# Optimization experiments

Hardware: AMD Instinct MI355X
Metric: run time of the kernel (lower is better)

## Reference

```python
import jax, jax.numpy as jnp
import numpy as np

B, T, D, H, LAT = 64, 512, 128, 512, 128


def setup_inputs() -> dict:
    key = jax.random.key(0)
    ks = jax.random.split(key, 17)
    s = lambda k, shape: (jax.random.normal(k, shape, jnp.float32) * 0.05)
    return {
        "padded_input": jax.random.normal(ks[0], (B, T, D), jnp.float32),
        "lengths": jnp.full((B,), T, jnp.int32),  # full lengths: packed == padded
        "W_ih_f": s(ks[1], (4 * H, D)), "W_hh_f": s(ks[2], (4 * H, H)), "b_f": s(ks[3], (4 * H,)),
        "W_ih_b": s(ks[4], (4 * H, D)), "W_hh_b": s(ks[5], (4 * H, H)), "b_b": s(ks[6], (4 * H,)),
        "W_ih_d": s(ks[7], (4 * H, D)), "W_hh_d": s(ks[8], (4 * H, H)), "b_d": s(ks[9], (4 * H,)),
        "W_lat": s(ks[10], (LAT, 4 * H)), "b_lat": s(ks[11], (LAT,)),
        "W_l2h": s(ks[12], (H, LAT)), "b_l2h": s(ks[13], (H,)),
        "W_out": s(ks[14], (D, H)), "b_out": s(ks[15], (D,)),
        "skip_alpha": jnp.asarray(0.5, jnp.float32),
    }


def _lstm(x, W_ih, W_hh, b, h0, c0):
    # x: [B, T, Din]; PyTorch gate order i, f, g, o; b = b_ih + b_hh pre-summed.
    xg = jnp.einsum('btd,gd->tbg', x, W_ih) + b  # [T, B, 4H], input GEMM hoisted out of scan

    def step(carry, xg_t):
        h, c = carry
        g = xg_t + h @ W_hh.T
        i, f, gc, o = jnp.split(g, 4, axis=-1)
        c = jax.nn.sigmoid(f) * c + jax.nn.sigmoid(i) * jnp.tanh(gc)
        h = jax.nn.sigmoid(o) * jnp.tanh(c)
        return (h, c), h

    (hT, cT), ys = jax.lax.scan(step, (h0, c0), xg)
    return jnp.transpose(ys, (1, 0, 2)), hT, cT  # [B, T, H], final h, final c


def reference(padded_input, lengths, W_ih_f, W_hh_f, b_f, W_ih_b, W_hh_b, b_b,
              W_ih_d, W_hh_d, b_d, W_lat, b_lat, W_l2h, b_l2h, W_out, b_out, skip_alpha):
    Bz, Tz, _ = padded_input.shape
    dt = padded_input.dtype
    z0 = jnp.zeros((Bz, H), dt)

    # Bidirectional encoder (single layer)
    out_f, hf, _ = _lstm(padded_input, W_ih_f, W_hh_f, b_f, z0, z0)
    out_b_rev, hb, _ = _lstm(padded_input[:, ::-1, :], W_ih_b, W_hh_b, b_b, z0, z0)
    out_b = out_b_rev[:, ::-1, :]
    enc_out = jnp.concatenate([out_f, out_b], axis=-1)  # [B, T, 2H]
    h_cat = jnp.concatenate([hf, hb], axis=-1)          # [B, 2H]

    # Masked mean pooling over valid timesteps
    mask = (jnp.arange(Tz)[None, :] < lengths[:, None]).astype(dt)[..., None]
    mean_hidden = (enc_out * mask).sum(axis=1) / lengths[:, None].astype(dt)
    latent_input = jnp.concatenate([h_cat, mean_hidden], axis=-1)  # [B, 4H]
    latent = latent_input @ W_lat.T + b_lat

    # Decoder init from latent; c0 = zeros
    h_dec = latent @ W_l2h.T + b_l2h

    # Teacher forcing with ratio 1.0, eval dropout, no noise:
    # per-step loop == one LSTM over padded_input[:, :T-1]
    dec_in = padded_input[:, :Tz - 1, :]
    y, _, _ = _lstm(dec_in, W_ih_d, W_hh_d, b_d, h_dec, jnp.zeros_like(h_dec))
    decoded = jnp.einsum('bth,dh->btd', y, W_out) + b_out  # [B, T-1, D]

    alpha = jax.nn.sigmoid(skip_alpha)
    return alpha * decoded + (1.0 - alpha) * padded_input[:, 1:, :]
```

## Files before the change

kernel.cpp:

```cpp
#include <hip/hip_runtime.h>
#include <cstdint>
#include <cstddef>

typedef __attribute__((ext_vector_type(8))) short bf16x8;
typedef __attribute__((ext_vector_type(4))) float f32x4;
typedef __attribute__((ext_vector_type(4))) unsigned u32x4;
typedef __attribute__((ext_vector_type(2))) unsigned u32x2;
typedef unsigned short ushort_t;

constexpr int kB = 64;
constexpr int kT = 512;
constexpr int kD = 128;
constexpr int kH = 512;
constexpr int kLat = 128;

constexpr size_t OFF_Y   = 0;
constexpr size_t Y_EL    = (size_t)(kT - 1) * kH * kB;
constexpr size_t OFF_XBF = OFF_Y + Y_EL;
constexpr size_t XBF_F   = (size_t)kT * kB * kD / 2;
constexpr size_t OFF_HT  = OFF_XBF + XBF_F;
constexpr size_t HT_F    = 3 * 2 * 32768 / 2;
constexpr size_t OFF_RDY = OFF_HT + HT_F;
constexpr size_t RDY_I   = 3 * 512 * 32;
constexpr size_t OFF_HFF = OFF_RDY + RDY_I;
constexpr size_t OFF_HFB = OFF_HFF + 32768;
constexpr size_t OFF_HSF = OFF_HFB + 32768;
constexpr size_t OFF_HSB = OFF_HSF + 32768;
constexpr size_t NEED_BYTES = (OFF_HSB + 32768) * 4;

#define MFMA_B16(A, Bv, C) C = __builtin_amdgcn_mfma_f32_16x16x32_bf16(A, Bv, C, 0, 0, 0)

__device__ __forceinline__ float sigf(float x) { return 1.0f / (1.0f + __expf(-x)); }
__device__ __forceinline__ float tanh_(float x) {
  float xc = fminf(fmaxf(x, -15.f), 15.f);
  float e = __expf(2.f * xc);
  return (e - 1.f) / (e + 1.f);
}
__device__ __forceinline__ ushort_t f2bf(float f) {
  unsigned u = __float_as_uint(f);
  u = (u + 0x7FFFu + ((u >> 16) & 1u)) >> 16;
  return (ushort_t)u;
}
__device__ __forceinline__ bf16x8 pack8(float4 a, float4 b) {
  bf16x8 v;
  v[0] = (short)f2bf(a.x); v[1] = (short)f2bf(a.y);
  v[2] = (short)f2bf(a.z); v[3] = (short)f2bf(a.w);
  v[4] = (short)f2bf(b.x); v[5] = (short)f2bf(b.y);
  v[6] = (short)f2bf(b.z); v[7] = (short)f2bf(b.w);
  return v;
}
__device__ __forceinline__ float cellup(const f32x4 a, float& c) {
  float ig = sigf(a[0]), fg = sigf(a[1]), gg = tanh_(a[2]), og = sigf(a[3]);
  c = fg * c + ig * gg;
  return og * tanh_(c);
}

__device__ __forceinline__ u32x4 llc_load_b128(const void* p) {
  u32x4 v;
  asm volatile("global_load_dwordx4 %0, %1, off sc0 sc1"
               : "=v"(v) : "v"(p) : "memory");
  return v;
}
__device__ __forceinline__ void llc_store_b64(void* p, u32x2 v) {
  asm volatile("global_store_dwordx2 %0, %1, off sc0 sc1"
               :: "v"(p), "v"(v) : "memory");
}
__device__ __forceinline__ void llc_store_b32(void* p, unsigned v) {
  asm volatile("global_store_dword %0, %1, off sc0 sc1"
               :: "v"(p), "v"(v) : "memory");
}
__device__ __forceinline__ void wait_vm0() {
  asm volatile("s_waitcnt vmcnt(0)" ::: "memory");
  __builtin_amdgcn_sched_barrier(0);
}

__global__ __launch_bounds__(256) void xbf_k(const float* __restrict__ X,
                                             ushort_t* __restrict__ xbf) {
  const int t = blockIdx.x, tid = threadIdx.x;
  const int b = tid >> 2, dq = (tid & 3) * 32;
  const float* src = X + ((size_t)b * kT + t) * kD + dq;
  ushort_t* dst = xbf + ((size_t)t * kB + b) * kD + dq;
  #pragma unroll
  for (int i = 0; i < 32; i += 8) {
    float4 u0 = *(const float4*)(src + i);
    float4 u1 = *(const float4*)(src + i + 4);
    *(bf16x8*)(dst + i) = pack8(u0, u1);
  }
}

__device__ __forceinline__ void xproj(const ushort_t* xb0, int q, const bf16x8* Ax,
                                      f32x4& a0, f32x4& a1, f32x4& a2, f32x4& a3,
                                      int b0n, int b1n, int b2n, int b3n) {
  #pragma unroll
  for (int ks = 0; ks < 4; ++ks) {
    const int ko = ks * 32 + q * 8;
    bf16x8 x0 = *(const bf16x8*)(xb0 + b0n * 128 + ko);
    bf16x8 x1 = *(const bf16x8*)(xb0 + b1n * 128 + ko);
    bf16x8 x2 = *(const bf16x8*)(xb0 + b2n * 128 + ko);
    bf16x8 x3 = *(const bf16x8*)(xb0 + b3n * 128 + ko);
    MFMA_B16(Ax[ks], x0, a0);
    MFMA_B16(Ax[ks], x1, a1);
    MFMA_B16(Ax[ks], x2, a2);
    MFMA_B16(Ax[ks], x3, a3);
  }
}

template<int MODE>
__global__ __launch_bounds__(256, 1) void lstm_k(
    const float* __restrict__ WhhA, const float* __restrict__ WhhB,
    const float* __restrict__ WihA, const float* __restrict__ WihB,
    const float* __restrict__ biaA, const float* __restrict__ biaB,
    const int* __restrict__ lengths, const ushort_t* __restrict__ xbf,
    float* __restrict__ ws) {
  __shared__ ushort_t hlds[32768];
  __shared__ ushort_t hx[64 * 20];
  const int tid = threadIdx.x;
  const int bid = blockIdx.x;
  const bool fwd = (MODE == 1) ? true : (bid < 32);
  const int gl = (MODE == 1) ? bid : (bid & 31);
  const float* Whh = fwd ? WhhA : WhhB;
  const float* Wih = fwd ? WihA : WihB;
  const float* bia = fwd ? biaA : biaB;
  const int dir_off = (MODE == 1) ? 2 : (fwd ? 0 : 1);
  ushort_t* hT = (ushort_t*)(ws + OFF_HT) + dir_off * 65536;
  unsigned* rdyf = (unsigned*)(ws + OFF_RDY) + (size_t)dir_off * 512 * 32;
  const int TS = (MODE == 1) ? (kT - 1) : kT;

  const int w = tid >> 6, lane = tid & 63;
  const int q = lane >> 4, r = lane & 15;
  const int JB = gl * 16;
  const int j4 = JB + 4 * w;
  const int gate = r & 3, jj = j4 + (r >> 2);

  bf16x8 Ah[16], Ax[4];
  {
    const float* p = Whh + ((size_t)(gate * kH + jj)) * kH + q * 8;
    #pragma unroll
    for (int ks = 0; ks < 16; ++ks)
      Ah[ks] = pack8(*(const float4*)(p + ks * 32), *(const float4*)(p + ks * 32 + 4));
    const float* px = Wih + ((size_t)(gate * kH + jj)) * kD + q * 8;
    #pragma unroll
    for (int ks = 0; ks < 4; ++ks)
      Ax[ks] = pack8(*(const float4*)(px + ks * 32), *(const float4*)(px + ks * 32 + 4));
  }
  const int jq = j4 + q;
  f32x4 bias_v;
  bias_v[0] = bia[0 * kH + jq];
  bias_v[1] = bia[1 * kH + jq];
  bias_v[2] = bia[2 * kH + jq];
  bias_v[3] = bia[3 * kH + jq];
  const int b0n = r, b1n = 16 + r, b2n = 32 + r, b3n = 48 + r;
  int len0 = 0, len1 = 0, len2 = 0, len3 = 0;
  if (MODE == 0) {
    len0 = lengths[b0n]; len1 = lengths[b1n];
    len2 = lengths[b2n]; len3 = lengths[b3n];
  }
  float c0 = 0.f, c1 = 0.f, c2 = 0.f, c3 = 0.f;
  float hs0 = 0.f, hs1 = 0.f, hs2 = 0.f, hs3 = 0.f;
  f32x4 a0 = bias_v, a1 = bias_v, a2 = bias_v, a3 = bias_v;
  {
    const int tx = fwd ? 0 : (kT - 1);
    xproj(xbf + (size_t)tx * 8192, q, Ax, a0, a1, a2, a3, b0n, b1n, b2n, b3n);
  }
  char* lp = (char*)hlds;
  float* yout = ws + OFF_Y;

  for (int t = 0; t < TS; ++t) {
    const bool do_rec = (MODE == 1) || (t > 0);
    if (do_rec) {
      if (t > 0) {
        const unsigned* fp = rdyf + (size_t)t * 32 + (lane & 31);
        for (;;) {
          unsigned v;
          asm volatile("global_load_dword %0, %1, off sc0 sc1"
                       : "=v"(v) : "v"(fp) : "memory");
          asm volatile("s_waitcnt vmcnt(0)" ::: "memory");
          if (__ballot(v != 0u) == ~0ull) break;
          __builtin_amdgcn_s_sleep(1);
        }
        __builtin_amdgcn_sched_barrier(0);
      }
      {
        const char* hsrc = (const char*)(hT + (t & 1) * 32768);
        u32x4 reg[16];
        #pragma unroll
        for (int i = 0; i < 16; ++i) {
          const int idx = tid + i * 256;
          reg[i] = llc_load_b128(hsrc + (size_t)idx * 16);
        }
        wait_vm0();
        #pragma unroll
        for (int i = 0; i < 16; ++i) {
          const int idx = tid + i * 256;
          const int bb = idx >> 6, cc = idx & 63;
          *(u32x4*)(lp + (((bb << 10) + (cc << 4)) ^ ((bb & 7) << 4))) = reg[i];
        }
      }
      __syncthreads();
      #pragma unroll
      for (int ks = 0; ks < 16; ++ks) {
        const int kb = ks * 64 + (q << 4);
        bf16x8 v0 = *(const bf16x8*)(lp + (((b0n << 10) + kb) ^ ((b0n & 7) << 4)));
        bf16x8 v1 = *(const bf16x8*)(lp + (((b1n << 10) + kb) ^ ((b1n & 7) << 4)));
        bf16x8 v2 = *(const bf16x8*)(lp + (((b2n << 10) + kb) ^ ((b2n & 7) << 4)));
        bf16x8 v3 = *(const bf16x8*)(lp + (((b3n << 10) + kb) ^ ((b3n & 7) << 4)));
        MFMA_B16(Ah[ks], v0, a0);
        MFMA_B16(Ah[ks], v1, a1);
        MFMA_B16(Ah[ks], v2, a2);
        MFMA_B16(Ah[ks], v3, a3);
      }
    }
    const float h0v = cellup(a0, c0);
    const float h1v = cellup(a1, c1);
    const float h2v = cellup(a2, c2);
    const float h3v = cellup(a3, c3);

    if (t < TS - 1) {
      const int jl = 4 * w + q;
      hx[b0n * 20 + jl] = f2bf(h0v);
      hx[b1n * 20 + jl] = f2bf(h1v);
      hx[b2n * 20 + jl] = f2bf(h2v);
      hx[b3n * 20 + jl] = f2bf(h3v);
      __syncthreads();
      {
        const int bb = tid >> 2, c4 = (tid & 3) * 4;
        u32x2 v = *(const u32x2*)&hx[bb * 20 + c4];
        llc_store_b64(hT + ((t + 1) & 1) * 32768 + bb * 512 + JB + c4, v);
      }
      __syncthreads();
      if (tid == 0) llc_store_b32(rdyf + (size_t)(t + 1) * 32 + gl, 1u);
    }
    if (MODE == 0) {
      const bool m0 = fwd ? (t < len0) : (t >= kT - len0);
      const bool m1 = fwd ? (t < len1) : (t >= kT - len1);
      const bool m2 = fwd ? (t < len2) : (t >= kT - len2);
      const bool m3 = fwd ? (t < len3) : (t >= kT - len3);
      hs0 += m0 ? h0v : 0.f;
      hs1 += m1 ? h1v : 0.f;
      hs2 += m2 ? h2v : 0.f;
      hs3 += m3 ? h3v : 0.f;
    } else {
      yout[((size_t)t * kH + jq) * kB + b0n] = h0v;
      yout[((size_t)t * kH + jq) * kB + b1n] = h1v;
      yout[((size_t)t * kH + jq) * kB + b2n] = h2v;
      yout[((size_t)t * kH + jq) * kB + b3n] = h3v;
    }
    if (t < TS - 1) {
      a0 = bias_v; a1 = bias_v; a2 = bias_v; a3 = bias_v;
      const int txn = fwd ? (t + 1) : (kT - 1 - (t + 1));
      xproj(xbf + (size_t)txn * 8192, q, Ax, a0, a1, a2, a3, b0n, b1n, b2n, b3n);
    } else if (MODE == 0) {
      float* hfin = ws + (fwd ? OFF_HFF : OFF_HFB);
      float* hsum = ws + (fwd ? OFF_HSF : OFF_HSB);
      hfin[jq * kB + b0n] = h0v; hfin[jq * kB + b1n] = h1v;
      hfin[jq * kB + b2n] = h2v; hfin[jq * kB + b3n] = h3v;
      hsum[jq * kB + b0n] = hs0; hsum[jq * kB + b1n] = hs1;
      hsum[jq * kB + b2n] = hs2; hsum[jq * kB + b3n] = hs3;
    }
  }
}

__global__ __launch_bounds__(256) void latent_k(
    const float* __restrict__ W_lat, const float* __restrict__ b_lat,
    const float* __restrict__ W_l2h, const float* __restrict__ b_l2h,
    const int* __restrict__ lengths, float* __restrict__ ws) {
  __shared__ __align__(16) float li[4 * kH];
  __shared__ __align__(16) float ls[kLat];
  const int b = blockIdx.x;
  const int tid = threadIdx.x;
  const float invlen = 1.0f / (float)lengths[b];
  for (int j = tid; j < kH; j += 256) {
    li[j]          = ws[OFF_HFF + (size_t)j * kB + b];
    li[kH + j]     = ws[OFF_HFB + (size_t)j * kB + b];
    li[2 * kH + j] = ws[OFF_HSF + (size_t)j * kB + b] * invlen;
    li[3 * kH + j] = ws[OFF_HSB + (size_t)j * kB + b] * invlen;
  }
  __syncthreads();
  if (tid < kLat) {
    const float* wv = W_lat + (size_t)tid * (4 * kH);
    float a = b_lat[tid];
    for (int k = 0; k < 4 * kH; k += 4) {
      const float4 w4 = *(const float4*)(wv + k);
      a += w4.x * li[k] + w4.y * li[k + 1] + w4.z * li[k + 2] + w4.w * li[k + 3];
    }
    ls[tid] = a;
  }
  __syncthreads();
  ushort_t* hTd = (ushort_t*)(ws + OFF_HT) + 2 * 65536;
  for (int j = tid; j < kH; j += 256) {
    const float* wv = W_l2h + (size_t)j * kLat;
    float a = b_l2h[j];
    #pragma unroll
    for (int k = 0; k < kLat; k += 4) {
      const float4 w4 = *(const float4*)(wv + k);
      a += w4.x * ls[k] + w4.y * ls[k + 1] + w4.z * ls[k + 2] + w4.w * ls[k + 3];
    }
    hTd[b * kH + j] = f2bf(a);
  }
}

__global__ __launch_bounds__(256) void out_k(
    const float* __restrict__ X, const float* __restrict__ W_out,
    const float* __restrict__ b_out, const float* __restrict__ alpha_p,
    const float* __restrict__ ws, float* __restrict__ out) {
  __shared__ __align__(16) float ys[128 * 64];
  __shared__ __align__(16) float Wo[128 * 128];
  const int t = blockIdx.x;
  const float* y = ws + OFF_Y + (size_t)t * kH * kB;
  const int tid = threadIdx.x;
  float acc[8][4];
  #pragma unroll
  for (int i = 0; i < 8; ++i)
    #pragma unroll
    for (int jj = 0; jj < 4; ++jj) acc[i][jj] = 0.f;
  const int tg = tid >> 4, tb = tid & 15;
  const int d0 = tg * 8, b0 = tb * 4;
  for (int ch = 0; ch < 4; ++ch) {
    __syncthreads();
    {
      const float4* s4 = (const float4*)(y + ch * 128 * 64);
      float4* d4 = (float4*)ys;
      #pragma unroll
      for (int i = 0; i < 8; ++i) d4[tid + i * 256] = s4[tid + i * 256];
    }
    {
      const int d = tid & 127, k0 = (tid >> 7) * 64;
      const float* src = W_out + (size_t)d * kH + ch * 128 + k0;
      #pragma unroll
      for (int i = 0; i < 64; i += 4) {
        float4 v = *(const float4*)(src + i);
        Wo[(k0 + i + 0) * 128 + d] = v.x;
        Wo[(k0 + i + 1) * 128 + d] = v.y;
        Wo[(k0 + i + 2) * 128 + d] = v.z;
        Wo[(k0 + i + 3) * 128 + d] = v.w;
      }
    }
    __syncthreads();
    #pragma unroll 2
    for (int k = 0; k < 128; ++k) {
      const float4 yv = *(const float4*)&ys[k * 64 + b0];
      const float4 w0 = *(const float4*)&Wo[k * 128 + d0];
      const float4 w1 = *(const float4*)&Wo[k * 128 + d0 + 4];
      const float wv[8] = {w0.x, w0.y, w0.z, w0.w, w1.x, w1.y, w1.z, w1.w};
      const float ya[4] = {yv.x, yv.y, yv.z, yv.w};
      #pragma unroll
      for (int di = 0; di < 8; ++di)
        #pragma unroll
        for (int bi = 0; bi < 4; ++bi)
          acc[di][bi] += wv[di] * ya[bi];
    }
  }
  const float alpha = sigf(alpha_p[0]);
  const float beta = 1.0f - alpha;
  #pragma unroll
  for (int bi = 0; bi < 4; ++bi) {
    const int b = b0 + bi;
    const float* xrow = X + ((size_t)b * kT + t + 1) * kD + d0;
    float* orow = out + ((size_t)b * (kT - 1) + t) * kD + d0;
    #pragma unroll
    for (int di = 0; di < 8; di += 4) {
      const float4 xv = *(const float4*)(xrow + di);
      float4 o;
      o.x = alpha * (acc[di + 0][bi] + b_out[d0 + di + 0]) + beta * xv.x;
      o.y = alpha * (acc[di + 1][bi] + b_out[d0 + di + 1]) + beta * xv.y;
      o.z = alpha * (acc[di + 2][bi] + b_out[d0 + di + 2]) + beta * xv.z;
      o.w = alpha * (acc[di + 3][bi] + b_out[d0 + di + 3]) + beta * xv.w;
      *(float4*)(orow + di) = o;
    }
  }
}

__global__ __launch_bounds__(256) void fallback_k(
    const float* __restrict__ X, const float* __restrict__ alpha_p,
    float* __restrict__ out, int n) {
  const int o = blockIdx.x * 256 + threadIdx.x;
  if (o >= n) return;
  const float alpha = sigf(alpha_p[0]);
  const int b = o / ((kT - 1) * kD);
  const int rr = o % ((kT - 1) * kD);
  const int t = rr / kD, d = rr % kD;
  out[o] = (1.0f - alpha) * X[((size_t)b * kT + t + 1) * kD + d];
}

extern "C" void kernel_launch(void* const* d_in, const int* in_sizes, int n_in,
                              void* d_out, int out_size, void* d_ws, size_t ws_size,
                              hipStream_t stream) {
  const float* X      = (const float*)d_in[0];
  const int*   lens   = (const int*)  d_in[1];
  const float* W_ih_f = (const float*)d_in[2];
  const float* W_hh_f = (const float*)d_in[3];
  const float* b_f    = (const float*)d_in[4];
  const float* W_ih_b = (const float*)d_in[5];
  const float* W_hh_b = (const float*)d_in[6];
  const float* b_b    = (const float*)d_in[7];
  const float* W_ih_d = (const float*)d_in[8];
  const float* W_hh_d = (const float*)d_in[9];
  const float* b_d    = (const float*)d_in[10];
  const float* W_lat  = (const float*)d_in[11];
  const float* b_lat  = (const float*)d_in[12];
  const float* W_l2h  = (const float*)d_in[13];
  const float* b_l2h  = (const float*)d_in[14];
  const float* W_out  = (const float*)d_in[15];
  const float* b_out  = (const float*)d_in[16];
  const float* alpha  = (const float*)d_in[17];
  float* ws  = (float*)d_ws;
  float* out = (float*)d_out;

  if (ws_size < NEED_BYTES) {
    fallback_k<<<(out_size + 255) / 256, 256, 0, stream>>>(X, alpha, out, out_size);
    return;
  }

  hipMemsetAsync((void*)(ws + OFF_HT), 0, (HT_F + RDY_I) * sizeof(float), stream);

  ushort_t* xbf = (ushort_t*)(ws + OFF_XBF);
  xbf_k<<<kT, 256, 0, stream>>>(X, xbf);
  lstm_k<0><<<64, 256, 0, stream>>>(W_hh_f, W_hh_b, W_ih_f, W_ih_b, b_f, b_b,
                                    lens, xbf, ws);
  latent_k<<<64, 256, 0, stream>>>(W_lat, b_lat, W_l2h, b_l2h, lens, ws);
  lstm_k<1><<<32, 256, 0, stream>>>(W_hh_d, nullptr, W_ih_d, nullptr, b_d, nullptr,
                                    lens, xbf, ws);
  out_k<<<kT - 1, 256, 0, stream>>>(X, W_out, b_out, alpha, ws, out);
}
```

Before: 5.704 ms.

## Replace block-level h staging and barriers with per-wave shuffles and per-wave ready flags

Each wave now transposes its new hidden-state values across lanes with ds_bpermute and stores them straight to the global h buffer. This removes the shared-memory staging array and the two __syncthreads per step. Readiness is now signalled with one flag per wave (128 flags per step instead of 32), so consumers poll twice as many flags with two loads per lane. The goal is to shorten the critical path of the cross-block recurrence handoff, at the cost of more flag traffic and polling.

Measured after the change: 6.056 ms. 6.2% more time.

```diff
diff --git a/kernel.cpp b/kernel.cpp
--- a/kernel.cpp
+++ b/kernel.cpp
@@ -21,7 +21,7 @@
 constexpr size_t OFF_HT  = OFF_XBF + XBF_F;
 constexpr size_t HT_F    = 3 * 2 * 32768 / 2;
 constexpr size_t OFF_RDY = OFF_HT + HT_F;
-constexpr size_t RDY_I   = 3 * 512 * 32;
+constexpr size_t RDY_I   = 3 * 512 * 128;
 constexpr size_t OFF_HFF = OFF_RDY + RDY_I;
 constexpr size_t OFF_HFB = OFF_HFF + 32768;
 constexpr size_t OFF_HSF = OFF_HFB + 32768;
@@ -36,11 +36,12 @@
   float e = __expf(2.f * xc);
   return (e - 1.f) / (e + 1.f);
 }
-__device__ __forceinline__ ushort_t f2bf(float f) {
+__device__ __forceinline__ unsigned f2bfu(float f) {
   unsigned u = __float_as_uint(f);
   u = (u + 0x7FFFu + ((u >> 16) & 1u)) >> 16;
-  return (ushort_t)u;
-}
+  return u & 0xFFFFu;
+}
+__device__ __forceinline__ ushort_t f2bf(float f) { return (ushort_t)f2bfu(f); }
 __device__ __forceinline__ bf16x8 pack8(float4 a, float4 b) {
   bf16x8 v;
   v[0] = (short)f2bf(a.x); v[1] = (short)f2bf(a.y);
@@ -113,7 +114,6 @@
     const int* __restrict__ lengths, const ushort_t* __restrict__ xbf,
     float* __restrict__ ws) {
   __shared__ ushort_t hlds[32768];
-  __shared__ ushort_t hx[64 * 20];
   const int tid = threadIdx.x;
   const int bid = blockIdx.x;
   const bool fwd = (MODE == 1) ? true : (bid < 32);
@@ -123,7 +123,7 @@
   const float* bia = fwd ? biaA : biaB;
   const int dir_off = (MODE == 1) ? 2 : (fwd ? 0 : 1);
   ushort_t* hT = (ushort_t*)(ws + OFF_HT) + dir_off * 65536;
-  unsigned* rdyf = (unsigned*)(ws + OFF_RDY) + (size_t)dir_off * 512 * 32;
+  unsigned* rdyf = (unsigned*)(ws + OFF_RDY) + (size_t)dir_off * 512 * 128;
   const int TS = (MODE == 1) ? (kT - 1) : kT;
 
   const int w = tid >> 6, lane = tid & 63;
@@ -164,18 +164,26 @@
   }
   char* lp = (char*)hlds;
   float* yout = ws + OFF_Y;
+  const int bp0 = ((0 << 4) | (lane & 15)) << 2;
+  const int bp1 = ((1 << 4) | (lane & 15)) << 2;
+  const int bp2 = ((2 << 4) | (lane & 15)) << 2;
+  const int bp3 = ((3 << 4) | (lane & 15)) << 2;
+  const bool selHi32 = (lane & 32) != 0;
+  const bool selHi16 = (lane & 16) != 0;
 
   for (int t = 0; t < TS; ++t) {
     const bool do_rec = (MODE == 1) || (t > 0);
     if (do_rec) {
       if (t > 0) {
-        const unsigned* fp = rdyf + (size_t)t * 32 + (lane & 31);
+        const unsigned* fp = rdyf + (size_t)t * 128;
         for (;;) {
-          unsigned v;
-          asm volatile("global_load_dword %0, %1, off sc0 sc1"
-                       : "=v"(v) : "v"(fp) : "memory");
+          unsigned v1, v2;
+          asm volatile("global_load_dword %0, %2, off sc0 sc1\n\t"
+                       "global_load_dword %1, %3, off sc0 sc1"
+                       : "=v"(v1), "=v"(v2)
+                       : "v"(fp + lane), "v"(fp + 64 + lane) : "memory");
           asm volatile("s_waitcnt vmcnt(0)" ::: "memory");
-          if (__ballot(v != 0u) == ~0ull) break;
+          if (__ballot((v1 != 0u) && (v2 != 0u)) == ~0ull) break;
           __builtin_amdgcn_s_sleep(1);
         }
         __builtin_amdgcn_sched_barrier(0);
@@ -216,19 +224,32 @@
     const float h3v = cellup(a3, c3);
 
     if (t < TS - 1) {
-      const int jl = 4 * w + q;
-      hx[b0n * 20 + jl] = f2bf(h0v);
-      hx[b1n * 20 + jl] = f2bf(h1v);
-      hx[b2n * 20 + jl] = f2bf(h2v);
-      hx[b3n * 20 + jl] = f2bf(h3v);
-      __syncthreads();
-      {
-        const int bb = tid >> 2, c4 = (tid & 3) * 4;
-        u32x2 v = *(const u32x2*)&hx[bb * 20 + c4];
-        llc_store_b64(hT + ((t + 1) & 1) * 32768 + bb * 512 + JB + c4, v);
-      }
-      __syncthreads();
-      if (tid == 0) llc_store_b32(rdyf + (size_t)(t + 1) * 32 + gl, 1u);
+      const int pk01 = (int)(f2bfu(h0v) | (f2bfu(h1v) << 16));
+      const int pk23 = (int)(f2bfu(h2v) | (f2bfu(h3v) << 16));
+      int r01_0 = __builtin_amdgcn_ds_bpermute(bp0, pk01);
+      int r23_0 = __builtin_amdgcn_ds_bpermute(bp0, pk23);
+      int r01_1 = __builtin_amdgcn_ds_bpermute(bp1, pk01);
+      int r23_1 = __builtin_amdgcn_ds_bpermute(bp1, pk23);
+      int r01_2 = __builtin_amdgcn_ds_bpermute(bp2, pk01);
+      int r23_2 = __builtin_amdgcn_ds_bpermute(bp2, pk23);
+      int r01_3 = __builtin_amdgcn_ds_bpermute(bp3, pk01);
+      int r23_3 = __builtin_amdgcn_ds_bpermute(bp3, pk23);
+      unsigned s0 = (unsigned)(selHi32 ? r23_0 : r01_0);
+      unsigned s1 = (unsigned)(selHi32 ? r23_1 : r01_1);
+      unsigned s2 = (unsigned)(selHi32 ? r23_2 : r01_2);
+      unsigned s3 = (unsigned)(selHi32 ? r23_3 : r01_3);
+      unsigned e0 = selHi16 ? (s0 >> 16) : (s0 & 0xFFFFu);
+      unsigned e1 = selHi16 ? (s1 >> 16) : (s1 & 0xFFFFu);
+      unsigned e2 = selHi16 ? (s2 >> 16) : (s2 & 0xFFFFu);
+      unsigned e3 = selHi16 ? (s3 >> 16) : (s3 & 0xFFFFu);
+      u32x2 hv;
+      hv[0] = e0 | (e1 << 16);
+      hv[1] = e2 | (e3 << 16);
+      ushort_t* dst = hT + ((t + 1) & 1) * 32768 + (size_t)lane * 512 + j4;
+      llc_store_b64(dst, hv);
+      asm volatile("s_waitcnt vmcnt(0)" ::: "memory");
+      if (lane == 0)
+        llc_store_b32(rdyf + (size_t)(t + 1) * 128 + gl * 4 + w, 1u);
     }
     if (MODE == 0) {
       const bool m0 = fwd ? (t < len0) : (t >= kT - len0);
```
